# Kernel tuning notes

Hardware: AMD Instinct MI355X
Metric: run time of the kernel (lower is better)

The kernel has to match this reference:

```python
import jax, jax.numpy as jnp
import numpy as np

T, B, L = 8192, 8, 1024
HID, H, KV, D = 2048, 16, 8, 128
G = H // KV
EPS = 1e-6
SCALE = 1.0 / float(np.sqrt(D))


def _rms(x, w):
    # RMSNorm over last dim (head_dim), eps=1e-6
    return x * jax.lax.rsqrt(jnp.mean(x * x, axis=-1, keepdims=True) + EPS) * w


def _rot_half(x):
    h = x.shape[-1] // 2
    return jnp.concatenate([-x[..., h:], x[..., :h]], axis=-1)


def setup_inputs() -> dict:
    key = jax.random.key(0)
    ks = jax.random.split(key, 12)
    inp = {}
    inp["packed_sequence"] = jax.random.normal(ks[0], (T, HID), jnp.float32)
    # rotary embeddings: per-sample positions 0..L-1, packed
    pos = jnp.tile(jnp.arange(L), B).astype(jnp.float32)
    inv = 1.0 / (10000.0 ** (jnp.arange(0, D, 2, dtype=jnp.float32) / D))
    fr = pos[:, None] * inv[None, :]
    emb = jnp.concatenate([fr, fr], axis=-1)  # [T, D]
    inp["cos"] = jnp.cos(emb)
    inp["sin"] = jnp.sin(emb)
    # per-sample causal float mask (additive): 0 allowed, -1e9 masked
    tril = jnp.tril(jnp.ones((L, L), bool))
    inp["attention_mask"] = jnp.broadcast_to(
        jnp.where(tril, 0.0, -1e9).astype(jnp.float32)[None], (B, L, L)
    )
    # disjoint und/gen routing indexes covering all T tokens
    inp["und_idx"] = jnp.arange(0, T, 2, dtype=jnp.int32)
    inp["gen_idx"] = jnp.arange(1, T, 2, dtype=jnp.int32)
    s = 0.02

    def lin(k, o, i):
        return jax.random.normal(k, (o, i), jnp.float32) * s

    kk = jax.random.split(ks[1], 8)
    inp["Wq_u"] = lin(kk[0], H * D, HID); inp["bq_u"] = jnp.zeros((H * D,), jnp.float32)
    inp["Wk_u"] = lin(kk[1], KV * D, HID); inp["bk_u"] = jnp.zeros((KV * D,), jnp.float32)
    inp["Wv_u"] = lin(kk[2], KV * D, HID); inp["bv_u"] = jnp.zeros((KV * D,), jnp.float32)
    inp["Wo_u"] = lin(kk[3], HID, H * D)
    inp["Wq_g"] = lin(kk[4], H * D, HID); inp["bq_g"] = jnp.zeros((H * D,), jnp.float32)
    inp["Wk_g"] = lin(kk[5], KV * D, HID); inp["bk_g"] = jnp.zeros((KV * D,), jnp.float32)
    inp["Wv_g"] = lin(kk[6], KV * D, HID); inp["bv_g"] = jnp.zeros((KV * D,), jnp.float32)
    inp["Wo_g"] = lin(kk[7], HID, H * D)
    inp["qn_u"] = jnp.ones((D,), jnp.float32); inp["kn_u"] = jnp.ones((D,), jnp.float32)
    inp["qn_g"] = jnp.ones((D,), jnp.float32); inp["kn_g"] = jnp.ones((D,), jnp.float32)
    return inp


def reference(packed_sequence, cos, sin, attention_mask, und_idx, gen_idx,
              Wq_u, bq_u, Wk_u, bk_u, Wv_u, bv_u, Wo_u,
              Wq_g, bq_g, Wk_g, bk_g, Wv_g, bv_g, Wo_g,
              qn_u, kn_u, qn_g, kn_g):
    x_u = packed_sequence[und_idx]  # [T/2, HID]
    x_g = packed_sequence[gen_idx]

    def route(Wu, bu, Wg, bg, width):
        out = jnp.zeros((T, width), packed_sequence.dtype)
        out = out.at[und_idx].set(x_u @ Wu.T + bu)
        out = out.at[gen_idx].set(x_g @ Wg.T + bg)
        return out

    q = route(Wq_u, bq_u, Wq_g, bq_g, H * D).reshape(T, H, D)
    k = route(Wk_u, bk_u, Wk_g, bk_g, KV * D).reshape(T, KV, D)
    v = route(Wv_u, bv_u, Wv_g, bv_g, KV * D).reshape(T, KV, D)

    # routed per-head QK RMSNorm (separate und/gen weights)
    qn = jnp.zeros_like(q).at[und_idx].set(_rms(q[und_idx], qn_u)).at[gen_idx].set(_rms(q[gen_idx], qn_g))
    kn = jnp.zeros_like(k).at[und_idx].set(_rms(k[und_idx], kn_u)).at[gen_idx].set(_rms(k[gen_idx], kn_g))

    c, s = cos[:, None, :], sin[:, None, :]  # unsqueeze_dim=1
    q = qn * c + _rot_half(qn) * s
    k = kn * c + _rot_half(kn) * s

    # GQA expansion: kv head i -> heads i*G..i*G+G-1
    k = jnp.repeat(k, G, axis=1)  # [T, H, D]
    v = jnp.repeat(v, G, axis=1)

    qb = q.reshape(B, L, H, D)
    kb = k.reshape(B, L, H, D)
    vb = v.reshape(B, L, H, D)

    scores = jnp.einsum('blhd,bmhd->bhlm', qb, kb) * SCALE
    scores = scores + attention_mask[:, None, :, :]
    p = jax.nn.softmax(scores, axis=-1)
    o = jnp.einsum('bhlm,bmhd->blhd', p, vb).reshape(T, H * D)

    out = jnp.zeros((T, HID), packed_sequence.dtype)
    out = out.at[und_idx].set(o[und_idx] @ Wo_u.T)
    out = out.at[gen_idx].set(o[gen_idx] @ Wo_g.T)
    return out
```

## Files before the change

### kernel.cpp

```cpp
#include <hip/hip_runtime.h>
#include <hip/hip_bf16.h>
#include <stdint.h>
#include <math.h>

#define T_TOK 8192
#define HID   2048
#define NH    16
#define NKV   8
#define HD    128
#define LSEQ  1024
#define BATCH 8
#define QKV_N 4096
#define KDIM  2048
#define NT64  32
#define SCALE 0.08838834764831845f

typedef __hip_bfloat16 bf16;
typedef __bf16 bf16x8 __attribute__((ext_vector_type(8)));
typedef float  f32x4  __attribute__((ext_vector_type(4)));

typedef const void __attribute__((address_space(1)))* gas_ptr;
typedef void       __attribute__((address_space(3)))* las_ptr;

__device__ __forceinline__ float b2f(bf16 x) { return __bfloat162float(x); }
__device__ __forceinline__ bf16  f2b(float x) { return __float2bfloat16(x); }
__device__ __forceinline__ unsigned short f2u(float x) {
    union { bf16 b; unsigned short u; } c; c.b = __float2bfloat16(x); return c.u;
}

__device__ __forceinline__ bf16x8 ld16(const void* p) {
    union { uint4 u; bf16x8 v; } c;
    c.u = *reinterpret_cast<const uint4*>(p);
    return c.v;
}

__device__ __forceinline__ void cp16(void* lds, const void* g) {
    __builtin_amdgcn_global_load_lds((gas_ptr)g, (las_ptr)lds, 16, 0, 0);
}

#define DSR(dst, base, imm) \
    asm volatile("ds_read_b128 %0, %1 offset:" #imm : "=v"(dst) : "v"(base))
#define SCHEDB() __builtin_amdgcn_sched_barrier(0)
#define LGKM0()  asm volatile("s_waitcnt lgkmcnt(0)")
#define MFMA16(a_, b_, c_) __builtin_amdgcn_mfma_f32_16x16x32_bf16(a_, b_, c_, 0, 0, 0)

__global__ __launch_bounds__(256) void k_f2b(const float* __restrict__ in,
                                             bf16* __restrict__ out, int n) {
    int i = blockIdx.x * blockDim.x + threadIdx.x;
    int stride = gridDim.x * blockDim.x;
    const float4* in4 = (const float4*)in;
    ushort4* out4 = (ushort4*)out;
    int n4 = n >> 2;
    for (int j = i; j < n4; j += stride) {
        float4 v = in4[j];
        ushort4 o;
        o.x = f2u(v.x); o.y = f2u(v.y); o.z = f2u(v.z); o.w = f2u(v.w);
        out4[j] = o;
    }
}

__global__ __launch_bounds__(256) void k_mod(const int* __restrict__ und,
                                             const int* __restrict__ gen,
                                             int* __restrict__ mod, int n) {
    int i = blockIdx.x * blockDim.x + threadIdx.x;
    if (i < n) { mod[und[i]] = 0; mod[gen[i]] = 1; }
}

template<int EPI>
__global__ __launch_bounds__(512)
void k_g201(const bf16* __restrict__ A,
            const bf16* __restrict__ Bw_u, const bf16* __restrict__ Bw_g,
            const int* __restrict__ und, const int* __restrict__ gen,
            const float* __restrict__ bq_u, const float* __restrict__ bk_u,
            const float* __restrict__ bv_u,
            const float* __restrict__ bq_g, const float* __restrict__ bk_g,
            const float* __restrict__ bv_g,
            bf16* __restrict__ outB, float* __restrict__ outF) {
    extern __shared__ char smem[];

    int modg = blockIdx.y;
    const bf16* Bw = modg ? Bw_g : Bw_u;
    const int* idx = modg ? gen : und;
    const float* bq = modg ? bq_g : bq_u;
    const float* bk = modg ? bk_g : bk_u;
    const float* bv = modg ? bv_g : bv_u;

    int gx = gridDim.x;
    int bid = blockIdx.x;
    int sw = (bid & 7) * (gx >> 3) + (bid >> 3);
    int tn = sw >> 4, tm = sw & 15;

    int tid = threadIdx.x;
    int w = tid >> 6, lane = tid & 63;
    int l16 = lane & 15, l4 = lane >> 4;
    int wm = w >> 2, wn = w & 3;

    int swzc = (tid & 3) ^ ((tid >> 3) & 3);
    const bf16* pA[2]; const bf16* pB[2];
#pragma unroll
    for (int j = 0; j < 2; ++j) {
        int row = j * 128 + (tid >> 2);
        pA[j] = A + (size_t)idx[tm * 256 + row] * KDIM + swzc * 8;
        pB[j] = Bw + (size_t)(tn * 256 + row) * KDIM + swzc * 8;
    }

    auto SU = [&](int t, int u, int kh) {
        char* dest = smem + (t & 1) * 65536 + u * 32768 + kh * 16384 + w * 1024;
        const bf16* const* p = u ? pB : pA;
        cp16(dest,        p[0] + t * 64 + kh * 32);
        cp16(dest + 8192, p[1] + t * 64 + kh * 32);
    };

    f32x4 acc[8][4];
#pragma unroll
    for (int m = 0; m < 8; ++m)
#pragma unroll
        for (int n = 0; n < 4; ++n) acc[m][n] = {0.f, 0.f, 0.f, 0.f};

    SU(0, 0, 0); SU(0, 1, 0); SU(0, 0, 1); SU(0, 1, 1);
    SU(1, 0, 0); SU(1, 1, 0);
    SCHEDB();
    asm volatile("s_waitcnt vmcnt(8)");
    __builtin_amdgcn_s_barrier();

    uint32_t cByte = (uint32_t)((l4 ^ ((l16 >> 1) & 3)) << 4);
    uint32_t aBase = (uint32_t)(wm * 128 + l16) * 64 + cByte;
    uint32_t bBase = 32768u + (uint32_t)(wn * 64 + l16) * 64 + cByte;

#define MROW(MI, XV) \
    acc[MI][0] = MFMA16(XV, b0, acc[MI][0]); \
    acc[MI][1] = MFMA16(XV, b1, acc[MI][1]); \
    acc[MI][2] = MFMA16(XV, b2, acc[MI][2]); \
    acc[MI][3] = MFMA16(XV, b3, acc[MI][3]);

#pragma unroll 1
    for (int t = 0; t < NT64; ++t) {
        char* buf = smem + (t & 1) * 65536;
        las_ptr aP = (las_ptr)(buf + aBase);
        las_ptr bP = (las_ptr)(buf + bBase);
        bf16x8 b0, b1, b2, b3, x0, x1, x2, x3;

        DSR(b0, bP, 0);    DSR(b1, bP, 1024);
        DSR(b2, bP, 2048); DSR(b3, bP, 3072);
        DSR(x0, aP, 0);    DSR(x1, aP, 1024);
        DSR(x2, aP, 2048); DSR(x3, aP, 3072);
        if (t + 1 < NT64) SU(t + 1, 0, 1);
        SCHEDB();
        __builtin_amdgcn_s_barrier();
        LGKM0(); SCHEDB();
        __builtin_amdgcn_s_setprio(1);
        MROW(0, x0) MROW(1, x1) MROW(2, x2) MROW(3, x3)
        __builtin_amdgcn_s_setprio(0);
        SCHEDB();
        __builtin_amdgcn_s_barrier();

        DSR(x0, aP, 4096); DSR(x1, aP, 5120);
        DSR(x2, aP, 6144); DSR(x3, aP, 7168);
        if (t + 1 < NT64) SU(t + 1, 1, 1);
        SCHEDB();
        if (t < NT64 - 1) asm volatile("s_waitcnt vmcnt(8)");
        else              asm volatile("s_waitcnt vmcnt(0)");
        __builtin_amdgcn_s_barrier();
        LGKM0(); SCHEDB();
        __builtin_amdgcn_s_setprio(1);
        MROW(4, x0) MROW(5, x1) MROW(6, x2) MROW(7, x3)
        __builtin_amdgcn_s_setprio(0);
        SCHEDB();
        __builtin_amdgcn_s_barrier();

        DSR(b0, bP, 16384); DSR(b1, bP, 17408);
        DSR(b2, bP, 18432); DSR(b3, bP, 19456);
        DSR(x0, aP, 16384); DSR(x1, aP, 17408);
        DSR(x2, aP, 18432); DSR(x3, aP, 19456);
        if (t + 2 < NT64) SU(t + 2, 0, 0);
        SCHEDB();
        __builtin_amdgcn_s_barrier();
        LGKM0(); SCHEDB();
        __builtin_amdgcn_s_setprio(1);
        MROW(0, x0) MROW(1, x1) MROW(2, x2) MROW(3, x3)
        __builtin_amdgcn_s_setprio(0);
        SCHEDB();
        __builtin_amdgcn_s_barrier();

        DSR(x0, aP, 20480); DSR(x1, aP, 21504);
        DSR(x2, aP, 22528); DSR(x3, aP, 23552);
        if (t + 2 < NT64) SU(t + 2, 1, 0);
        SCHEDB();
        if (t < NT64 - 2)       asm volatile("s_waitcnt vmcnt(8)");
        else if (t == NT64 - 2) asm volatile("s_waitcnt vmcnt(4)");
        else                    asm volatile("s_waitcnt vmcnt(0)");
        __builtin_amdgcn_s_barrier();
        LGKM0(); SCHEDB();
        __builtin_amdgcn_s_setprio(1);
        MROW(4, x0) MROW(5, x1) MROW(6, x2) MROW(7, x3)
        __builtin_amdgcn_s_setprio(0);
        SCHEDB();
        __builtin_amdgcn_s_barrier();
    }
#undef MROW

    int rowbase = tm * 256 + wm * 128;
    int colbase = tn * 256 + wn * 64;
#pragma unroll
    for (int m = 0; m < 8; ++m) {
#pragma unroll
        for (int r = 0; r < 4; ++r) {
            int row = rowbase + m * 16 + l4 * 4 + r;
            int token = idx[row];
#pragma unroll
            for (int n = 0; n < 4; ++n) {
                int col = colbase + n * 16 + l16;
                float v = acc[m][n][r];
                if (EPI == 0) {
                    float bias = (col < 2048) ? bq[col]
                               : (col < 3072) ? bk[col - 2048] : bv[col - 3072];
                    outB[(size_t)token * QKV_N + col] = f2b(v + bias);
                } else {
                    outF[(size_t)token * HID + col] = v;
                }
            }
        }
    }
}

__global__ __launch_bounds__(256)
void k_normrope(const bf16* __restrict__ qkv,
                const float* __restrict__ cosT, const float* __restrict__ sinT,
                const int* __restrict__ mod,
                const float* __restrict__ qn_u, const float* __restrict__ qn_g,
                const float* __restrict__ kn_u, const float* __restrict__ kn_g,
                bf16* __restrict__ Qo, bf16* __restrict__ Ko) {
    int t = blockIdx.x;
    int tid = threadIdx.x;
    int w = tid >> 6, lane = tid & 63;
    int m = mod[t];
    int b = t >> 10, pos = t & 1023;
    const bf16* row = qkv + (size_t)t * QKV_N;
    int d0 = 2 * lane, d1 = 2 * lane + 1;
    float c0 = cosT[(size_t)t * HD + d0], c1 = cosT[(size_t)t * HD + d1];
    float s0 = sinT[(size_t)t * HD + d0], s1 = sinT[(size_t)t * HD + d1];
    float sgn = (lane < 32) ? -1.f : 1.f;
    const float* qw = m ? qn_g : qn_u;
    const float* kw = m ? kn_g : kn_u;

    for (int u = w; u < 24; u += 4) {
        float v0 = b2f(row[u * HD + d0]);
        float v1 = b2f(row[u * HD + d1]);
        float ss = v0 * v0 + v1 * v1;
#pragma unroll
        for (int msk = 1; msk < 64; msk <<= 1) ss += __shfl_xor(ss, msk);
        float rs = rsqrtf(ss * (1.0f / HD) + 1e-6f);
        const float* wsc = (u < 16) ? qw : kw;
        float n0 = v0 * rs * wsc[d0], n1 = v1 * rs * wsc[d1];
        float o0 = __shfl_xor(n0, 32), o1 = __shfl_xor(n1, 32);
        float r0 = n0 * c0 + sgn * o0 * s0;
        float r1 = n1 * c1 + sgn * o1 * s1;
        if (u < 16) {
            size_t o = ((size_t)(b * NH + u) * LSEQ + pos) * HD;
            Qo[o + d0] = f2b(r0); Qo[o + d1] = f2b(r1);
        } else {
            size_t o = ((size_t)(b * NKV + (u - 16)) * LSEQ + pos) * HD;
            Ko[o + d0] = f2b(r0); Ko[o + d1] = f2b(r1);
        }
    }
}

__global__ __launch_bounds__(256)
void k_vt(const bf16* __restrict__ qkv, bf16* __restrict__ Vt) {
    __shared__ bf16 lds[64][72];
    int bk = blockIdx.x;
    int b = bk >> 3, kv = bk & 7;
    int pos0 = blockIdx.y * 64;
    int d0 = blockIdx.z * 64;
    int tid = threadIdx.x;

#pragma unroll
    for (int it = 0; it < 2; ++it) {
        int c = tid + it * 256;
        int row = c >> 3, col8 = (c & 7) * 8;
        const bf16* src = qkv + (size_t)(b * LSEQ + pos0 + row) * QKV_N
                        + 3072 + kv * HD + d0 + col8;
        *reinterpret_cast<uint4*>(&lds[row][col8]) = *reinterpret_cast<const uint4*>(src);
    }
    __syncthreads();

#pragma unroll
    for (int it = 0; it < 2; ++it) {
        int c = tid + it * 256;
        int drow = c & 63, pos8 = (c >> 6) * 8;
        union { unsigned short s[8]; uint4 u; } g;
#pragma unroll
        for (int j = 0; j < 8; ++j)
            g.s[j] = *reinterpret_cast<const unsigned short*>(&lds[pos8 + j][drow]);
        bf16* dst = Vt + ((size_t)bk * HD + d0 + drow) * LSEQ + pos0 + pos8;
        *reinterpret_cast<uint4*>(dst) = g.u;
    }
}

__global__ __launch_bounds__(256)
void k_attn(const bf16* __restrict__ Q, const bf16* __restrict__ K,
            const bf16* __restrict__ Vt, bf16* __restrict__ O) {
    int bid = blockIdx.x;
    int p = bid & 3;
    int h = (bid >> 2) & 15;
    int b = bid >> 6;
    int tid = threadIdx.x;
    int w = tid >> 6, lane = tid & 63;
    int l16 = lane & 15, l4 = lane >> 4;
    int j = p * 4 + w;

    const bf16* qhb = Q + (size_t)(b * NH + h) * LSEQ * HD;
    int kv = h >> 1;
    const bf16* kb = K + (size_t)(b * NKV + kv) * LSEQ * HD;
    const bf16* vtb = Vt + (size_t)(b * NKV + kv) * HD * LSEQ;

    __shared__ bf16 Pl[4][32][72];

    f32x4 zero = {0.f, 0.f, 0.f, 0.f};

#pragma unroll 1
    for (int half = 0; half < 2; ++half) {
        int rowblk = half ? (31 - j) : j;
        int q0 = rowblk * 32;
        int kend = q0 + 32;

        bf16x8 qf[2][4];
#pragma unroll
        for (int rf = 0; rf < 2; ++rf)
#pragma unroll
            for (int c = 0; c < 4; ++c)
                qf[rf][c] = ld16(qhb + (size_t)(q0 + rf * 16 + l16) * HD + c * 32 + l4 * 8);

        f32x4 oacc[2][8];
#pragma unroll
        for (int rf = 0; rf < 2; ++rf)
#pragma unroll
            for (int d = 0; d < 8; ++d) oacc[rf][d] = zero;
        float mr[2][4], lr[2][4];
#pragma unroll
        for (int rf = 0; rf < 2; ++rf)
#pragma unroll
            for (int r = 0; r < 4; ++r) { mr[rf][r] = -INFINITY; lr[rf][r] = 0.f; }

        for (int kt = 0; kt < kend; kt += 64) {
            f32x4 s[2][4];
#pragma unroll
            for (int rf = 0; rf < 2; ++rf)
#pragma unroll
                for (int kf = 0; kf < 4; ++kf) s[rf][kf] = zero;
#pragma unroll
            for (int c = 0; c < 4; ++c) {
                bf16x8 kf4[4];
#pragma unroll
                for (int kf = 0; kf < 4; ++kf)
                    kf4[kf] = ld16(kb + (size_t)(kt + kf * 16 + l16) * HD + c * 32 + l4 * 8);
#pragma unroll
                for (int rf = 0; rf < 2; ++rf)
#pragma unroll
                    for (int kf = 0; kf < 4; ++kf)
                        s[rf][kf] = MFMA16(qf[rf][c], kf4[kf], s[rf][kf]);
            }
#pragma unroll
            for (int rf = 0; rf < 2; ++rf) {
#pragma unroll
                for (int r = 0; r < 4; ++r) {
                    int qrow = q0 + rf * 16 + l4 * 4 + r;
                    float sc[4];
                    float rm = -1e30f;
#pragma unroll
                    for (int kf = 0; kf < 4; ++kf) {
                        int key = kt + kf * 16 + l16;
                        sc[kf] = (key <= qrow) ? s[rf][kf][r] * SCALE : -1e30f;
                        rm = fmaxf(rm, sc[kf]);
                    }
#pragma unroll
                    for (int msk = 1; msk < 16; msk <<= 1) rm = fmaxf(rm, __shfl_xor(rm, msk));
                    float mn = fmaxf(mr[rf][r], rm);
                    float corr = __expf(mr[rf][r] - mn);
                    mr[rf][r] = mn;
                    float rsum = 0.f;
#pragma unroll
                    for (int kf = 0; kf < 4; ++kf) {
                        float pv = __expf(sc[kf] - mn);
                        rsum += pv;
                        Pl[w][rf * 16 + l4 * 4 + r][kf * 16 + l16] = f2b(pv);
                    }
#pragma unroll
                    for (int msk = 1; msk < 16; msk <<= 1) rsum += __shfl_xor(rsum, msk);
                    lr[rf][r] = lr[rf][r] * corr + rsum;
#pragma unroll
                    for (int d = 0; d < 8; ++d) oacc[rf][d][r] *= corr;
                }
            }
            bf16x8 pf[2][2];
#pragma unroll
            for (int rf = 0; rf < 2; ++rf)
#pragma unroll
                for (int ks = 0; ks < 2; ++ks)
                    pf[rf][ks] = ld16(&Pl[w][rf * 16 + l16][ks * 32 + l4 * 8]);
#pragma unroll
            for (int dt = 0; dt < 8; ++dt) {
#pragma unroll
                for (int ks = 0; ks < 2; ++ks) {
                    bf16x8 vfr = ld16(vtb + (size_t)(dt * 16 + l16) * LSEQ + kt + ks * 32 + l4 * 8);
#pragma unroll
                    for (int rf = 0; rf < 2; ++rf)
                        oacc[rf][dt] = MFMA16(pf[rf][ks], vfr, oacc[rf][dt]);
                }
            }
        }

#pragma unroll
        for (int rf = 0; rf < 2; ++rf)
#pragma unroll
            for (int r = 0; r < 4; ++r) lr[rf][r] = 1.0f / lr[rf][r];
        int trow = b * LSEQ + q0;
#pragma unroll
        for (int rf = 0; rf < 2; ++rf)
#pragma unroll
            for (int dt = 0; dt < 8; ++dt)
#pragma unroll
                for (int r = 0; r < 4; ++r) {
                    int t = trow + rf * 16 + l4 * 4 + r;
                    O[(size_t)t * HID + h * HD + dt * 16 + l16] = f2b(oacc[rf][dt][r] * lr[rf][r]);
                }
    }
}

extern "C" void kernel_launch(void* const* d_in, const int* in_sizes, int n_in,
                              void* d_out, int out_size, void* d_ws, size_t ws_size,
                              hipStream_t stream) {
    const float* x    = (const float*)d_in[0];
    const float* cosT = (const float*)d_in[1];
    const float* sinT = (const float*)d_in[2];
    const int* und = (const int*)d_in[4];
    const int* gen = (const int*)d_in[5];
    const float* Wq_u = (const float*)d_in[6];
    const float* bq_u = (const float*)d_in[7];
    const float* Wk_u = (const float*)d_in[8];
    const float* bk_u = (const float*)d_in[9];
    const float* Wv_u = (const float*)d_in[10];
    const float* bv_u = (const float*)d_in[11];
    const float* Wo_u = (const float*)d_in[12];
    const float* Wq_g = (const float*)d_in[13];
    const float* bq_g = (const float*)d_in[14];
    const float* Wk_g = (const float*)d_in[15];
    const float* bk_g = (const float*)d_in[16];
    const float* Wv_g = (const float*)d_in[17];
    const float* bv_g = (const float*)d_in[18];
    const float* Wo_g = (const float*)d_in[19];
    const float* qn_u = (const float*)d_in[20];
    const float* kn_u = (const float*)d_in[21];
    const float* qn_g = (const float*)d_in[22];
    const float* kn_g = (const float*)d_in[23];
    float* out = (float*)d_out;

    char* ws = (char*)d_ws;
    size_t off = 0;
    auto alloc = [&](size_t bytes) -> void* {
        void* p = ws + off;
        off += (bytes + 255) & ~(size_t)255;
        return p;
    };
    bf16* xb      = (bf16*)alloc((size_t)T_TOK * HID * 2);
    bf16* Wqkv_u  = (bf16*)alloc((size_t)QKV_N * KDIM * 2);
    bf16* Wqkv_g  = (bf16*)alloc((size_t)QKV_N * KDIM * 2);
    bf16* Wob_u   = (bf16*)alloc((size_t)HID * HID * 2);
    bf16* Wob_g   = (bf16*)alloc((size_t)HID * HID * 2);
    int*  mod     = (int*)alloc((size_t)T_TOK * 4);
    bf16* qkv     = (bf16*)alloc((size_t)T_TOK * QKV_N * 2);
    bf16* Qa      = (bf16*)alloc((size_t)BATCH * NH  * LSEQ * HD * 2);
    bf16* Ka      = (bf16*)alloc((size_t)BATCH * NKV * LSEQ * HD * 2);
    bf16* Vt      = (bf16*)alloc((size_t)BATCH * NKV * HD * LSEQ * 2);
    bf16* Ob      = (bf16*)alloc((size_t)T_TOK * HID * 2);
    (void)ws_size; (void)in_sizes; (void)n_in; (void)out_size;

    (void)hipFuncSetAttribute((const void*)k_g201<0>,
                              hipFuncAttributeMaxDynamicSharedMemorySize, 131072);
    (void)hipFuncSetAttribute((const void*)k_g201<1>,
                              hipFuncAttributeMaxDynamicSharedMemorySize, 131072);

    k_f2b<<<1024, 256, 0, stream>>>(x, xb, T_TOK * HID);
    k_f2b<<<1024, 256, 0, stream>>>(Wq_u, Wqkv_u,               2048 * 2048);
    k_f2b<<<1024, 256, 0, stream>>>(Wk_u, Wqkv_u + 2048 * 2048, 1024 * 2048);
    k_f2b<<<1024, 256, 0, stream>>>(Wv_u, Wqkv_u + 3072 * 2048, 1024 * 2048);
    k_f2b<<<1024, 256, 0, stream>>>(Wq_g, Wqkv_g,               2048 * 2048);
    k_f2b<<<1024, 256, 0, stream>>>(Wk_g, Wqkv_g + 2048 * 2048, 1024 * 2048);
    k_f2b<<<1024, 256, 0, stream>>>(Wv_g, Wqkv_g + 3072 * 2048, 1024 * 2048);
    k_f2b<<<1024, 256, 0, stream>>>(Wo_u, Wob_u, 2048 * 2048);
    k_f2b<<<1024, 256, 0, stream>>>(Wo_g, Wob_g, 2048 * 2048);
    k_mod<<<16, 256, 0, stream>>>(und, gen, mod, T_TOK / 2);

    k_g201<0><<<dim3(16 * 16, 2), 512, 131072, stream>>>(
        xb, Wqkv_u, Wqkv_g, und, gen, bq_u, bk_u, bv_u, bq_g, bk_g, bv_g,
        qkv, nullptr);

    k_normrope<<<T_TOK, 256, 0, stream>>>(qkv, cosT, sinT, mod,
                                          qn_u, qn_g, kn_u, kn_g, Qa, Ka);
    k_vt<<<dim3(BATCH * NKV, LSEQ / 64, HD / 64), 256, 0, stream>>>(qkv, Vt);

    k_attn<<<BATCH * NH * 4, 256, 0, stream>>>(Qa, Ka, Vt, Ob);

    k_g201<1><<<dim3(8 * 16, 2), 512, 131072, stream>>>(
        Ob, Wob_u, Wob_g, und, gen, nullptr, nullptr, nullptr,
        nullptr, nullptr, nullptr, nullptr, out);
}
```

Before: 480.4 us.

## Merge conversion launches and prefetch V, exp2 softmax, MFMA priority in attention

Replaces the nine fp32-to-bf16 conversion launches and the routing-mask launch with a single launch that uses a 2D grid, one row per segment. In the attention loop, all V fragments for the tile are loaded at the start of the iteration so their latency overlaps the QK MFMAs and the softmax. The scale is folded with log2(e) so the softmax can use exp2f, and the MFMA sections are wrapped in s_setprio. Holding the prefetched V fragments increases register pressure, which could lower occupancy. Using 256 blocks per segment may give less parallelism than the old 1024-block launches.

```diff
diff --git a/kernel.cpp b/kernel.cpp
--- a/kernel.cpp
+++ b/kernel.cpp
@@ -13,7 +13,7 @@
 #define QKV_N 4096
 #define KDIM  2048
 #define NT64  32
-#define SCALE 0.08838834764831845f
+#define SC2   0.12752039376060341f
 
 typedef __hip_bfloat16 bf16;
 typedef __bf16 bf16x8 __attribute__((ext_vector_type(8)));
@@ -44,26 +44,32 @@
 #define LGKM0()  asm volatile("s_waitcnt lgkmcnt(0)")
 #define MFMA16(a_, b_, c_) __builtin_amdgcn_mfma_f32_16x16x32_bf16(a_, b_, c_, 0, 0, 0)
 
-__global__ __launch_bounds__(256) void k_f2b(const float* __restrict__ in,
-                                             bf16* __restrict__ out, int n) {
+struct F2BSeg { const float* src; bf16* dst; int n4; };
+struct F2BArgs {
+    F2BSeg s[9];
+    const int* und; const int* gen; int* mod; int nmod;
+};
+
+__global__ __launch_bounds__(256) void k_f2ball(F2BArgs A) {
+    int seg = blockIdx.y;
     int i = blockIdx.x * blockDim.x + threadIdx.x;
     int stride = gridDim.x * blockDim.x;
-    const float4* in4 = (const float4*)in;
-    ushort4* out4 = (ushort4*)out;
-    int n4 = n >> 2;
-    for (int j = i; j < n4; j += stride) {
+    if (seg == 9) {
+        for (int j = i; j < A.nmod; j += stride) {
+            A.mod[A.und[j]] = 0;
+            A.mod[A.gen[j]] = 1;
+        }
+        return;
+    }
+    F2BSeg sg = A.s[seg];
+    const float4* in4 = (const float4*)sg.src;
+    ushort4* out4 = (ushort4*)sg.dst;
+    for (int j = i; j < sg.n4; j += stride) {
         float4 v = in4[j];
         ushort4 o;
         o.x = f2u(v.x); o.y = f2u(v.y); o.z = f2u(v.z); o.w = f2u(v.w);
         out4[j] = o;
     }
-}
-
-__global__ __launch_bounds__(256) void k_mod(const int* __restrict__ und,
-                                             const int* __restrict__ gen,
-                                             int* __restrict__ mod, int n) {
-    int i = blockIdx.x * blockDim.x + threadIdx.x;
-    if (i < n) { mod[und[i]] = 0; mod[gen[i]] = 1; }
 }
 
 template<int EPI>
@@ -342,7 +348,16 @@
 #pragma unroll
             for (int r = 0; r < 4; ++r) { mr[rf][r] = -INFINITY; lr[rf][r] = 0.f; }
 
+#pragma unroll 1
         for (int kt = 0; kt < kend; kt += 64) {
+            bf16x8 vf[16];
+#pragma unroll
+            for (int dt = 0; dt < 8; ++dt)
+#pragma unroll
+                for (int ks = 0; ks < 2; ++ks)
+                    vf[dt * 2 + ks] = ld16(vtb + (size_t)(dt * 16 + l16) * LSEQ
+                                           + kt + ks * 32 + l4 * 8);
+
             f32x4 s[2][4];
 #pragma unroll
             for (int rf = 0; rf < 2; ++rf)
@@ -354,12 +369,15 @@
 #pragma unroll
                 for (int kf = 0; kf < 4; ++kf)
                     kf4[kf] = ld16(kb + (size_t)(kt + kf * 16 + l16) * HD + c * 32 + l4 * 8);
+                __builtin_amdgcn_s_setprio(1);
 #pragma unroll
                 for (int rf = 0; rf < 2; ++rf)
 #pragma unroll
                     for (int kf = 0; kf < 4; ++kf)
                         s[rf][kf] = MFMA16(qf[rf][c], kf4[kf], s[rf][kf]);
+                __builtin_amdgcn_s_setprio(0);
             }
+
 #pragma unroll
             for (int rf = 0; rf < 2; ++rf) {
 #pragma unroll
@@ -370,18 +388,18 @@
 #pragma unroll
                     for (int kf = 0; kf < 4; ++kf) {
                         int key = kt + kf * 16 + l16;
-                        sc[kf] = (key <= qrow) ? s[rf][kf][r] * SCALE : -1e30f;
+                        sc[kf] = (key <= qrow) ? s[rf][kf][r] * SC2 : -1e30f;
                         rm = fmaxf(rm, sc[kf]);
                     }
 #pragma unroll
                     for (int msk = 1; msk < 16; msk <<= 1) rm = fmaxf(rm, __shfl_xor(rm, msk));
                     float mn = fmaxf(mr[rf][r], rm);
-                    float corr = __expf(mr[rf][r] - mn);
+                    float corr = exp2f(mr[rf][r] - mn);
                     mr[rf][r] = mn;
                     float rsum = 0.f;
 #pragma unroll
                     for (int kf = 0; kf < 4; ++kf) {
-                        float pv = __expf(sc[kf] - mn);
+                        float pv = exp2f(sc[kf] - mn);
                         rsum += pv;
                         Pl[w][rf * 16 + l4 * 4 + r][kf * 16 + l16] = f2b(pv);
                     }
@@ -392,22 +410,22 @@
                     for (int d = 0; d < 8; ++d) oacc[rf][d][r] *= corr;
                 }
             }
+
             bf16x8 pf[2][2];
 #pragma unroll
             for (int rf = 0; rf < 2; ++rf)
 #pragma unroll
                 for (int ks = 0; ks < 2; ++ks)
                     pf[rf][ks] = ld16(&Pl[w][rf * 16 + l16][ks * 32 + l4 * 8]);
-#pragma unroll
-            for (int dt = 0; dt < 8; ++dt) {
-#pragma unroll
-                for (int ks = 0; ks < 2; ++ks) {
-                    bf16x8 vfr = ld16(vtb + (size_t)(dt * 16 + l16) * LSEQ + kt + ks * 32 + l4 * 8);
+            __builtin_amdgcn_s_setprio(1);
+#pragma unroll
+            for (int dt = 0; dt < 8; ++dt)
+#pragma unroll
+                for (int ks = 0; ks < 2; ++ks)
 #pragma unroll
                     for (int rf = 0; rf < 2; ++rf)
-                        oacc[rf][dt] = MFMA16(pf[rf][ks], vfr, oacc[rf][dt]);
-                }
-            }
+                        oacc[rf][dt] = MFMA16(pf[rf][ks], vf[dt * 2 + ks], oacc[rf][dt]);
+            __builtin_amdgcn_s_setprio(0);
         }
 
 #pragma unroll
@@ -480,16 +498,18 @@
     (void)hipFuncSetAttribute((const void*)k_g201<1>,
                               hipFuncAttributeMaxDynamicSharedMemorySize, 131072);
 
-    k_f2b<<<1024, 256, 0, stream>>>(x, xb, T_TOK * HID);
-    k_f2b<<<1024, 256, 0, stream>>>(Wq_u, Wqkv_u,               2048 * 2048);
-    k_f2b<<<1024, 256, 0, stream>>>(Wk_u, Wqkv_u + 2048 * 2048, 1024 * 2048);
-    k_f2b<<<1024, 256, 0, stream>>>(Wv_u, Wqkv_u + 3072 * 2048, 1024 * 2048);
-    k_f2b<<<1024, 256, 0, stream>>>(Wq_g, Wqkv_g,               2048 * 2048);
-    k_f2b<<<1024, 256, 0, stream>>>(Wk_g, Wqkv_g + 2048 * 2048, 1024 * 2048);
-    k_f2b<<<1024, 256, 0, stream>>>(Wv_g, Wqkv_g + 3072 * 2048, 1024 * 2048);
-    k_f2b<<<1024, 256, 0, stream>>>(Wo_u, Wob_u, 2048 * 2048);
-    k_f2b<<<1024, 256, 0, stream>>>(Wo_g, Wob_g, 2048 * 2048);
-    k_mod<<<16, 256, 0, stream>>>(und, gen, mod, T_TOK / 2);
+    F2BArgs fa;
+    fa.s[0] = { x,    xb,                  T_TOK * HID / 4 };
+    fa.s[1] = { Wq_u, Wqkv_u,              2048 * 2048 / 4 };
+    fa.s[2] = { Wk_u, Wqkv_u + 2048 * 2048, 1024 * 2048 / 4 };
+    fa.s[3] = { Wv_u, Wqkv_u + 3072 * 2048, 1024 * 2048 / 4 };
+    fa.s[4] = { Wq_g, Wqkv_g,              2048 * 2048 / 4 };
+    fa.s[5] = { Wk_g, Wqkv_g + 2048 * 2048, 1024 * 2048 / 4 };
+    fa.s[6] = { Wv_g, Wqkv_g + 3072 * 2048, 1024 * 2048 / 4 };
+    fa.s[7] = { Wo_u, Wob_u,               2048 * 2048 / 4 };
+    fa.s[8] = { Wo_g, Wob_g,               2048 * 2048 / 4 };
+    fa.und = und; fa.gen = gen; fa.mod = mod; fa.nmod = T_TOK / 2;
+    k_f2ball<<<dim3(256, 10), 256, 0, stream>>>(fa);
 
     k_g201<0><<<dim3(16 * 16, 2), 512, 131072, stream>>>(
         xb, Wqkv_u, Wqkv_g, und, gen, bq_u, bk_u, bv_u, bq_g, bk_g, bv_g,
```

Result: slower. 542.1 us (+12.8%).
